# Kernel tuning notes

Measured on AMD Instinct MI355X. Metric: run time of the kernel, lower is better.

## Reference

```python
import jax, jax.numpy as jnp
import numpy as np

DIM_V = 512
NUM_HEADS = 8
LN_EPS = 1e-5


def _layernorm(x):
    # LayerNorm over last dim, no affine (simplified_layer_norm=True)
    mu = jnp.mean(x, axis=-1, keepdims=True)
    var = jnp.mean(jnp.square(x - mu), axis=-1, keepdims=True)
    return (x - mu) * jax.lax.rsqrt(var + LN_EPS)


def setup_inputs() -> dict:
    key = jax.random.key(0)
    ks = jax.random.split(key, 12)
    B, Nq, Nk, dQ, dK, dV = 16, 1024, 1024, 512, 512, DIM_V
    s = 0.02
    return {
        "Q": jax.random.normal(ks[0], (B, Nq, dQ), jnp.float32),
        "K": jax.random.normal(ks[1], (B, Nk, dK), jnp.float32),
        "Wq": jax.random.normal(ks[2], (dQ, dV), jnp.float32) * s,
        "bq": jnp.zeros((dV,), jnp.float32),
        "Wk": jax.random.normal(ks[3], (dK, dV), jnp.float32) * s,
        "bk": jnp.zeros((dV,), jnp.float32),
        "Wv": jax.random.normal(ks[4], (dK, dV), jnp.float32) * s,
        "bv": jnp.zeros((dV,), jnp.float32),
        "Wo": jax.random.normal(ks[5], (dV, dV), jnp.float32) * s,
        "bo": jnp.zeros((dV,), jnp.float32),
    }


def reference(Q, K, Wq, bq, Wk, bk, Wv, bv, Wo, bo):
    H = NUM_HEADS
    dh = DIM_V // H
    q = Q @ Wq + bq            # [B, Nq, dV]
    k = K @ Wk + bk            # [B, Nk, dV]
    v = K @ Wv + bv            # [B, Nk, dV]
    B, Nq, _ = q.shape
    Nk = k.shape[1]
    qh = q.reshape(B, Nq, H, dh)
    kh = k.reshape(B, Nk, H, dh)
    vh = v.reshape(B, Nk, H, dh)
    # NOTE: faithful to source — scale by sqrt(dim_V), not sqrt(head_dim)
    scores = jnp.einsum('bqhd,bkhd->bhqk', qh, kh) / jnp.sqrt(jnp.asarray(DIM_V, q.dtype))
    A = jax.nn.softmax(scores, axis=-1)                    # [B, H, Nq, Nk]
    attn = jnp.einsum('bhqk,bkhd->bqhd', A, vh).reshape(B, Nq, DIM_V)
    O = q + attn               # residual with projected Q
    O = _layernorm(O)          # ln0 (no affine)
    O = O + jax.nn.gelu(O @ Wo + bo, approximate=False)
    O = _layernorm(O)          # ln1 (no affine)
    return O
```

## Files before the change

kernel.cpp:

```cpp
#include <hip/hip_runtime.h>
#include <hip/hip_bf16.h>
#include <math.h>

typedef __bf16 bf16;
typedef __bf16 bf16x8 __attribute__((ext_vector_type(8)));
typedef float  f32x4  __attribute__((ext_vector_type(4)));
typedef float  f32x16 __attribute__((ext_vector_type(16)));
typedef unsigned u32x4 __attribute__((ext_vector_type(4)));

#define MFMA16(a,b,c) __builtin_amdgcn_mfma_f32_16x16x32_bf16((a),(b),(c),0,0,0)
#define MFMA32(a,b,c) __builtin_amdgcn_mfma_f32_32x32x16_bf16((a),(b),(c),0,0,0)
#define KSCALE 0.0637587159f

__device__ __forceinline__ void async16p(const void* g, void* l) {
    __builtin_amdgcn_global_load_lds((const __attribute__((address_space(1))) void*)g,
                                     (__attribute__((address_space(3))) void*)l,
                                     16, 0, 0);
}

__device__ __forceinline__ float fexp2(float x) {
#if __has_builtin(__builtin_amdgcn_exp2f)
    return __builtin_amdgcn_exp2f(x);
#else
    return exp2f(x);
#endif
}

__device__ __forceinline__ unsigned pkbf(float a, float b) {
    union { bf16 h[2]; unsigned u; } x;
    x.h[0] = (bf16)a; x.h[1] = (bf16)b; return x.u;
}

__device__ __forceinline__ void plswap(unsigned &a, unsigned &b) {
#if __has_builtin(__builtin_amdgcn_permlane32_swap)
    auto r = __builtin_amdgcn_permlane32_swap((int)a, (int)b, false, false);
    a = (unsigned)r[0]; b = (unsigned)r[1];
#else
    unsigned sa = (unsigned)__shfl_xor((int)a, 32);
    unsigned sb = (unsigned)__shfl_xor((int)b, 32);
    bool hi = (threadIdx.x & 32) != 0;
    unsigned na = hi ? sb : a;
    unsigned nb = hi ? b  : sa;
    a = na; b = nb;
#endif
}

__global__ __launch_bounds__(256) void prep_w_kernel(
    const float* __restrict__ Wq, const float* __restrict__ Wk,
    const float* __restrict__ Wv, const float* __restrict__ Wo,
    bf16* __restrict__ WqT, bf16* __restrict__ WkT,
    bf16* __restrict__ WvT, bf16* __restrict__ WoT)
{
    __shared__ float tile[32][33];
    const int bx = blockIdx.x;
    const float* W; bf16* T;
    switch (bx >> 8) {
      case 0: W=Wq; T=WqT; break;
      case 1: W=Wk; T=WkT; break;
      case 2: W=Wv; T=WvT; break;
      default: W=Wo; T=WoT; break;
    }
    const int rest = bx & 255;
    const int k0 = (rest & 15) * 32, n0 = (rest >> 4) * 32;
    const int tx = threadIdx.x & 31, ty = threadIdx.x >> 5;
    #pragma unroll
    for (int i=0;i<32;i+=8)
        tile[ty+i][tx] = W[(size_t)(k0+ty+i)*512 + n0+tx];
    __syncthreads();
    #pragma unroll
    for (int i=0;i<32;i+=8)
        T[(size_t)(n0+ty+i)*512 + k0+tx] = (bf16)tile[tx][ty+i];
}

__global__ __launch_bounds__(256) void csum_kernel(
    const float* __restrict__ Wo, float* __restrict__ csum)
{
    const int n = blockIdx.x*256 + threadIdx.x;
    float s = 0.f;
    #pragma unroll 8
    for (int k=0;k<512;k++) s += Wo[(size_t)k*512 + n];
    csum[n] = s;
}

__global__ __launch_bounds__(256, 2) void gemm_proj_kernel(
    const float* __restrict__ Qf, const float* __restrict__ Kf,
    const bf16* __restrict__ WqT, const bf16* __restrict__ WkT,
    const bf16* __restrict__ WvT,
    const float* __restrict__ bq, const float* __restrict__ bk,
    const float* __restrict__ bv,
    bf16* __restrict__ qbb, bf16* __restrict__ kbb, bf16* __restrict__ vT)
{
    __shared__ __align__(16) char smem[65536];
    float* As32 = (float*)smem;
    bf16*  Bs   = (bf16*)(smem + 32768);
    bf16*  Lt   = (bf16*)smem;

    const int x = blockIdx.x;
    const bool isQ = (x < 256);
    int m0, n0;
    const float* A; const bf16 *BT0, *BT1; const float *bb0, *bb1;
    if (isQ) {
        m0 = (x >> 1) * 128; n0 = (x & 1) * 128;
        A = Qf; BT0 = WqT + (size_t)n0*512; BT1 = WqT + (size_t)(n0+256)*512;
        bb0 = bq + n0; bb1 = bq + n0 + 256;
    } else {
        int r = x - 256;
        m0 = (r >> 2) * 128; n0 = (r & 3) * 128;
        A = Kf; BT0 = WkT + (size_t)n0*512; BT1 = WvT + (size_t)n0*512;
        bb0 = bk + n0; bb1 = bv + n0;
    }

    const int tid = threadIdx.x;
    const int lane = tid & 63, wave = tid >> 6;
    const int qd = lane >> 4, lr = lane & 15;
    const int wm = (wave & 1) * 64, wn = (wave >> 1) * 64;

    const float* gA = A + (size_t)(m0 + (tid>>3))*512 + (((tid&7)^((tid>>3)&7))*4);
    const int bgr = ((tid & 3) ^ ((tid >> 3) & 3)) * 8;
    const bf16* gB0 = BT0 + (size_t)(tid>>2)*512 + bgr;
    const bf16* gB1 = BT1 + (size_t)(tid>>2)*512 + bgr;

    f32x4 acc[2][4][4];
    #pragma unroll
    for (int p=0;p<2;p++)
      #pragma unroll
      for (int i=0;i<4;i++)
        #pragma unroll
        for (int j=0;j<4;j++) acc[p][i][j] = (f32x4){0,0,0,0};

    auto stage = [&](int buf, int k0) {
        float* lA = As32 + buf*4096 + wave*256;
        #pragma unroll
        for (int i=0;i<4;i++)
            async16p(gA + k0 + (size_t)i*32*512, lA + i*1024);
        bf16* lB0 = Bs + buf*8192 + wave*512;
        async16p(gB0 + k0,                  lB0);
        async16p(gB0 + k0 + (size_t)64*512, lB0 + 2048);
        bf16* lB1 = Bs + buf*8192 + 4096 + wave*512;
        async16p(gB1 + k0,                  lB1);
        async16p(gB1 + k0 + (size_t)64*512, lB1 + 2048);
    };

    stage(0, 0);
    for (int t = 0; t < 16; ++t) {
        const int cur = t & 1;
        __builtin_amdgcn_sched_barrier(0);
        __builtin_amdgcn_s_barrier();
        if (t < 15) {
            stage(cur ^ 1, (t+1)*32);
            asm volatile("s_waitcnt vmcnt(8)" ::: "memory");
        } else {
            asm volatile("s_waitcnt vmcnt(0)" ::: "memory");
        }
        __builtin_amdgcn_s_barrier();

        const float* Ab = As32 + cur*4096;
        const bf16*  Bb = Bs   + cur*8192;
        bf16x8 af[4], bfr[2][4];
        #pragma unroll
        for (int mi=0;mi<4;mi++) {
            int row = wm + mi*16 + lr;
            f32x4 f0 = *(f32x4*)(Ab + row*32 + (((qd*2  )^(lr&7))*4));
            f32x4 f1 = *(f32x4*)(Ab + row*32 + (((qd*2+1)^(lr&7))*4));
            bf16x8 a;
            a[0]=(bf16)f0[0]; a[1]=(bf16)f0[1]; a[2]=(bf16)f0[2]; a[3]=(bf16)f0[3];
            a[4]=(bf16)f1[0]; a[5]=(bf16)f1[1]; a[6]=(bf16)f1[2]; a[7]=(bf16)f1[3];
            af[mi] = a;
        }
        #pragma unroll
        for (int p=0;p<2;p++)
          #pragma unroll
          for (int ni=0;ni<4;ni++)
            bfr[p][ni] = *(bf16x8*)(Bb + p*4096 + (wn+ni*16+lr)*32
                                       + ((qd^((lr>>1)&3))*8));
        #pragma unroll
        for (int p=0;p<2;p++)
          #pragma unroll
          for (int mi=0;mi<4;mi++)
            #pragma unroll
            for (int ni=0;ni<4;ni++)
              acc[p][mi][ni] = MFMA16(af[mi], bfr[p][ni], acc[p][mi][ni]);
    }

    if (isQ) {
        #pragma unroll
        for (int p=0;p<2;p++) {
            const float* bb = p ? bb1 : bb0;
            #pragma unroll
            for (int ni=0;ni<4;ni++) {
                int nl = wn + ni*16 + lr;
                int n = n0 + p*256 + nl;
                float bv0 = bb[nl];
                #pragma unroll
                for (int mi=0;mi<4;mi++) {
                    int mb = m0 + wm + mi*16 + qd*4;
                    #pragma unroll
                    for (int r=0;r<4;r++)
                        qbb[(size_t)(mb+r)*512 + n] = (bf16)(acc[p][mi][ni][r] + bv0);
                }
            }
        }
    } else {
        #pragma unroll
        for (int ni=0;ni<4;ni++) {
            int nl = wn + ni*16 + lr;
            int n = n0 + nl;
            float bv0 = bb0[nl];
            #pragma unroll
            for (int mi=0;mi<4;mi++) {
                int mb = m0 + wm + mi*16 + qd*4;
                #pragma unroll
                for (int r=0;r<4;r++)
                    kbb[(size_t)(mb+r)*512 + n] = (bf16)((acc[0][mi][ni][r] + bv0)*KSCALE);
            }
        }
        const int b = m0 >> 10, tok0 = m0 & 1023;
        const int row = tid >> 2, ch = tid & 3;
        #pragma unroll
        for (int half = 0; half < 2; ++half) {
            __syncthreads();
            if ((wn >> 6) == half) {
                #pragma unroll
                for (int ni=0;ni<4;ni++) {
                    int nl = ni*16 + lr;
                    float bvv = bb1[half*64 + nl];
                    #pragma unroll
                    for (int mi=0;mi<4;mi++)
                      #pragma unroll
                      for (int r=0;r<4;r++) {
                        int col = wm + mi*16 + qd*4 + r;
                        Lt[nl*128 + ((((col>>3)^(nl&7))<<3) | (col&7))]
                            = (bf16)(acc[1][mi][ni][r] + bvv);
                      }
                }
            }
            __syncthreads();
            const int h = (n0 >> 6) + half;
            bf16* dst = vT + ((size_t)((b*8 + h)*64 + row))*1024 + tok0 + ch*32;
            #pragma unroll
            for (int s=0;s<4;s++) {
                int g = (ch*4 + s) ^ (row & 7);
                *(uint4*)(dst + s*8) = *(uint4*)(Lt + row*128 + g*8);
            }
        }
    }
}

__global__ __launch_bounds__(256, 4) void attn_kernel(
    const bf16* __restrict__ qb, const bf16* __restrict__ kb,
    const bf16* __restrict__ vT, bf16* __restrict__ attnb)
{
    const int x = blockIdx.x;
    const int qt = x >> 7, h = x & 7, b = (x & 127) >> 3;
    const int tid = threadIdx.x, lane = tid & 63, wave = tid >> 6;
    const int l = lane & 31, hi = lane >> 5;
    const int q0w = qt*128 + wave*32;

    __shared__ __align__(16) bf16 kv[2][2][4096];
    __shared__ float ls[4][32];

    bf16x8 aq[4];
    {
        const bf16* qrow = qb + ((size_t)(b*1024 + q0w + l))*512 + h*64 + hi*8;
        #pragma unroll
        for (int st=0; st<4; ++st) aq[st] = *(const bf16x8*)(qrow + st*16);
    }

    const int srow = lane >> 3;
    const int sgA  = (lane & 7) ^ srow ^ wave;
    const int sgB  = sgA ^ 4;
    const bf16* kg0 = kb + ((size_t)(b*1024 + wave*8 + srow))*512      + h*64 + sgA*8;
    const bf16* kg1 = kb + ((size_t)(b*1024 + wave*8 + srow + 32))*512 + h*64 + sgB*8;
    const bf16* vg0 = vT + ((size_t)((b*8 + h)*64 + wave*8 + srow))*1024      + sgA*8;
    const bf16* vg1 = vT + ((size_t)((b*8 + h)*64 + wave*8 + srow + 32))*1024 + sgB*8;

    auto stage = [&](int buf, int t) {
        const size_t ko = (size_t)t*64*512;
        async16p(kg0 + ko,     &kv[buf][0][wave*512]);
        async16p(kg1 + ko,     &kv[buf][0][2048 + wave*512]);
        async16p(vg0 + t*64,   &kv[buf][1][wave*512]);
        async16p(vg1 + t*64,   &kv[buf][1][2048 + wave*512]);
    };

    f32x16 accO[2];
    accO[0] = (f32x16)0.f; accO[1] = (f32x16)0.f;
    float lsum = 0.f;
    const int kx = (l & 7) ^ (l >> 3);

    stage(0, 0);
    for (int t=0; t<16; ++t) {
        const int cur = t & 1;
        __builtin_amdgcn_sched_barrier(0);
        __builtin_amdgcn_s_barrier();
        if (t < 15) {
            stage(cur ^ 1, t + 1);
            asm volatile("s_waitcnt vmcnt(4)" ::: "memory");
        } else {
            asm volatile("s_waitcnt vmcnt(0)" ::: "memory");
        }
        __builtin_amdgcn_s_barrier();

        const bf16* Ks = kv[cur][0];
        const bf16* Vs = kv[cur][1];

        u32x4 paf[4];
        #pragma unroll
        for (int kb2=0; kb2<2; ++kb2) {
            f32x16 sT = (f32x16)0.f;
            __builtin_amdgcn_s_setprio(1);
            #pragma unroll
            for (int st=0; st<4; ++st) {
                bf16x8 kf = *(const bf16x8*)(Ks + (kb2*32 + l)*64
                               + (((st*2 + hi) ^ kx ^ (kb2<<2))*8));
                sT = MFMA32(kf, aq[st], sT);
            }
            __builtin_amdgcn_s_setprio(0);
            unsigned u[8];
            #pragma unroll
            for (int m=0; m<8; ++m) {
                float e0 = fexp2(sT[2*m]);
                float e1 = fexp2(sT[2*m+1]);
                lsum += e0 + e1;
                u[m] = pkbf(e0, e1);
            }
            #pragma unroll
            for (int sb=0; sb<2; ++sb) {
                unsigned a0=u[4*sb], a1=u[4*sb+1], a2=u[4*sb+2], a3=u[4*sb+3];
                plswap(a0, a2);
                plswap(a1, a3);
                paf[kb2*2 + sb] = (u32x4){a0, a1, a2, a3};
            }
        }
        __builtin_amdgcn_s_setprio(1);
        #pragma unroll
        for (int db=0; db<2; ++db) {
            f32x16 a = accO[db];
            #pragma unroll
            for (int st=0; st<4; ++st) {
                bf16x8 vf = *(const bf16x8*)(Vs + (db*32 + l)*64
                               + (((st*2 + hi) ^ kx ^ (db<<2))*8));
                u32x4 pp = paf[st];
                bf16x8 pf = *(bf16x8*)&pp;
                a = MFMA32(pf, vf, a);
            }
            accO[db] = a;
        }
        __builtin_amdgcn_s_setprio(0);
    }

    lsum += __shfl_xor(lsum, 32);
    ls[wave][l] = lsum;
    __syncthreads();

    #pragma unroll
    for (int g=0; g<4; ++g) {
        f32x4 lv = *(const f32x4*)(&ls[wave][g*8 + hi*4]);
        f32x4 inv;
        #pragma unroll
        for (int i=0;i<4;i++) inv[i] = 1.f / lv[i];
        #pragma unroll
        for (int db=0; db<2; ++db) {
            #pragma unroll
            for (int i=0;i<4;i++) {
                int r = g*4 + i;
                int qrow = q0w + g*8 + hi*4 + i;
                size_t idx = ((size_t)(b*1024 + qrow))*512 + h*64 + db*32 + l;
                float o = accO[db][r] * inv[i] + (float)qb[idx];
                attnb[idx] = (bf16)o;
            }
        }
    }
}

__global__ __launch_bounds__(256) void ln_stats_kernel(
    const bf16* __restrict__ attnb, float2* __restrict__ stats)
{
    const int wave = threadIdx.x >> 6, lane = threadIdx.x & 63;
    const int row = blockIdx.x*4 + wave;
    const size_t base = (size_t)row*512 + lane*8;
    bf16x8 av = *(const bf16x8*)(attnb + base);
    float x[8];
    #pragma unroll
    for (int i=0;i<8;i++) x[i] = (float)av[i];
    float s1 = 0.f, s2 = 0.f;
    #pragma unroll
    for (int i=0;i<8;i++){ s1 += x[i]; s2 += x[i]*x[i]; }
    #pragma unroll
    for (int off=1; off<64; off<<=1) { s1 += __shfl_xor(s1, off); s2 += __shfl_xor(s2, off); }
    float mu  = s1 * (1.f/512.f);
    float var = s2 * (1.f/512.f) - mu*mu;
    float rstd = rsqrtf(var + 1e-5f);
    if (lane == 0) stats[row] = make_float2(mu, rstd);
}

__global__ __launch_bounds__(256, 4) void gemm_o_kernel(
    const bf16* __restrict__ attnb, const bf16* __restrict__ WoT,
    const float* __restrict__ bo, const float* __restrict__ csum,
    const float2* __restrict__ stats, bf16* __restrict__ xb)
{
    __shared__ __align__(16) char smem[24576];
    bf16* As = (bf16*)smem;
    bf16* Bs = (bf16*)(smem + 8192);
    const int m0 = blockIdx.x * 64, n0 = blockIdx.y * 128;
    const int tid = threadIdx.x;
    const int lane = tid & 63, wave = tid >> 6;
    const int qd = lane >> 4, lr = lane & 15;
    const int wm = (wave & 1) * 32, wn = (wave >> 1) * 64;

    const int bgr = ((tid & 3) ^ ((tid >> 3) & 3)) * 8;
    const bf16* gA = attnb + (size_t)(m0 + (tid>>2))*512 + bgr;
    const bf16* gB = WoT   + (size_t)(n0 + (tid>>2))*512 + bgr;

    f32x4 acc[2][4];
    #pragma unroll
    for (int i=0;i<2;i++)
      #pragma unroll
      for (int j=0;j<4;j++) acc[i][j] = (f32x4){0,0,0,0};

    auto stage = [&](int buf, int k0) {
        async16p(gA + k0,                  As + buf*2048 + wave*512);
        bf16* lB = Bs + buf*4096 + wave*512;
        async16p(gB + k0,                  lB);
        async16p(gB + k0 + (size_t)64*512, lB + 2048);
    };

    stage(0, 0);
    for (int t = 0; t < 16; ++t) {
        const int cur = t & 1;
        __builtin_amdgcn_sched_barrier(0);
        __builtin_amdgcn_s_barrier();
        if (t < 15) {
            stage(cur ^ 1, (t+1)*32);
            asm volatile("s_waitcnt vmcnt(3)" ::: "memory");
        } else {
            asm volatile("s_waitcnt vmcnt(0)" ::: "memory");
        }
        __builtin_amdgcn_s_barrier();

        const bf16* Ab = As + cur*2048;
        const bf16* Bb = Bs + cur*4096;
        bf16x8 af[2], bfr[4];
        #pragma unroll
        for (int mi=0;mi<2;mi++)
            af[mi] = *(bf16x8*)(Ab + (wm+mi*16+lr)*32 + ((qd^((lr>>1)&3))*8));
        #pragma unroll
        for (int ni=0;ni<4;ni++)
            bfr[ni] = *(bf16x8*)(Bb + (wn+ni*16+lr)*32 + ((qd^((lr>>1)&3))*8));
        #pragma unroll
        for (int mi=0;mi<2;mi++)
          #pragma unroll
          for (int ni=0;ni<4;ni++)
            acc[mi][ni] = MFMA16(af[mi], bfr[ni], acc[mi][ni]);
    }

    float csn[4], bon[4];
    #pragma unroll
    for (int ni=0;ni<4;ni++) {
        int n = n0 + wn + ni*16 + lr;
        csn[ni] = csum[n];
        bon[ni] = bo[n];
    }
    #pragma unroll
    for (int mi=0;mi<2;mi++) {
        #pragma unroll
        for (int r=0;r<4;r++) {
            int row = m0 + wm + mi*16 + qd*4 + r;
            float2 st = stats[row];
            float mu = st.x, rstd = st.y;
            #pragma unroll
            for (int ni=0;ni<4;ni++) {
                int n = n0 + wn + ni*16 + lr;
                float g = rstd*acc[mi][ni][r] - rstd*mu*csn[ni] + bon[ni];
                float gelu = 0.5f * g * (1.f + erff(g * 0.70710678118654752f));
                size_t idx = (size_t)row*512 + n;
                float lnx = ((float)attnb[idx] - mu) * rstd;
                xb[idx] = (bf16)(lnx + gelu);
            }
        }
    }
}

__global__ __launch_bounds__(256) void ln1_kernel(
    const bf16* __restrict__ xb, float* __restrict__ out)
{
    const int wave = threadIdx.x >> 6, lane = threadIdx.x & 63;
    const int row = blockIdx.x*4 + wave;
    const size_t base = (size_t)row*512 + lane*8;
    bf16x8 xv = *(const bf16x8*)(xb + base);
    float x[8];
    #pragma unroll
    for (int i=0;i<8;i++) x[i] = (float)xv[i];
    float s1 = 0.f, s2 = 0.f;
    #pragma unroll
    for (int i=0;i<8;i++){ s1 += x[i]; s2 += x[i]*x[i]; }
    #pragma unroll
    for (int off=1; off<64; off<<=1) { s1 += __shfl_xor(s1, off); s2 += __shfl_xor(s2, off); }
    float mu  = s1 * (1.f/512.f);
    float var = s2 * (1.f/512.f) - mu*mu;
    float rstd = rsqrtf(var + 1e-5f);
    float4 o0 = {(x[0]-mu)*rstd,(x[1]-mu)*rstd,(x[2]-mu)*rstd,(x[3]-mu)*rstd};
    float4 o1 = {(x[4]-mu)*rstd,(x[5]-mu)*rstd,(x[6]-mu)*rstd,(x[7]-mu)*rstd};
    *(float4*)(out + base)     = o0;
    *(float4*)(out + base + 4) = o1;
}

extern "C" void kernel_launch(void* const* d_in, const int* in_sizes, int n_in,
                              void* d_out, int out_size, void* d_ws, size_t ws_size,
                              hipStream_t stream)
{
    (void)in_sizes; (void)n_in; (void)out_size; (void)ws_size;
    const float* Q  = (const float*)d_in[0];
    const float* K  = (const float*)d_in[1];
    const float* Wq = (const float*)d_in[2];
    const float* bq = (const float*)d_in[3];
    const float* Wk = (const float*)d_in[4];
    const float* bk = (const float*)d_in[5];
    const float* Wv = (const float*)d_in[6];
    const float* bv = (const float*)d_in[7];
    const float* Wo = (const float*)d_in[8];
    const float* bo = (const float*)d_in[9];
    float* out = (float*)d_out;

    const size_t nTok = (size_t)16*1024*512;
    char* p = (char*)d_ws;
    auto alloc = [&](size_t bytes)->char* {
        char* r = p; p += (bytes + 255) & ~(size_t)255; return r;
    };
    bf16*   WqT   = (bf16*)alloc(512*512*2);
    bf16*   WkT   = (bf16*)alloc(512*512*2);
    bf16*   WvT   = (bf16*)alloc(512*512*2);
    bf16*   WoT   = (bf16*)alloc(512*512*2);
    bf16*   qbb   = (bf16*)alloc(nTok*2);
    bf16*   kbb   = (bf16*)alloc(nTok*2);
    bf16*   vT    = (bf16*)alloc(nTok*2);
    bf16*   attnb = (bf16*)alloc(nTok*2);
    bf16*   xb    = (bf16*)alloc(nTok*2);
    float*  csum  = (float*)alloc(512*4);
    float2* stats = (float2*)alloc(16384*8);

    prep_w_kernel<<<1024, 256, 0, stream>>>(Wq, Wk, Wv, Wo, WqT, WkT, WvT, WoT);
    csum_kernel<<<2, 256, 0, stream>>>(Wo, csum);
    gemm_proj_kernel<<<768, 256, 0, stream>>>(Q, K, WqT, WkT, WvT,
                                              bq, bk, bv, qbb, kbb, vT);
    attn_kernel<<<dim3(1024), 256, 0, stream>>>(qbb, kbb, vT, attnb);
    ln_stats_kernel<<<4096, 256, 0, stream>>>(attnb, stats);
    gemm_o_kernel<<<dim3(256,4), 256, 0, stream>>>(attnb, WoT, bo, csum, stats, xb);
    ln1_kernel<<<4096, 256, 0, stream>>>(xb, out);
}
```

Baseline: 265.7 us.

## Fuse column-sum into weight prep and split projection GEMM into per-output tiles

The Wo column-sum kernel is folded into the weight transpose kernel using block reductions and atomicAdd, with a memset clearing the buffer first. The projection GEMM now computes a single 128x128 output tile per block over 1536 blocks instead of paired Q halves or K/V outputs. B fragments are read straight from global memory into registers, which halves LDS use and lets occupancy rise to three blocks per CU. In exchange, the fp32 activation tile is re-read for every output slice (K is loaded twice), and the B loads are no longer staged through LDS.

```diff
diff --git a/kernel.cpp b/kernel.cpp
--- a/kernel.cpp
+++ b/kernel.cpp
@@ -49,7 +49,8 @@
     const float* __restrict__ Wq, const float* __restrict__ Wk,
     const float* __restrict__ Wv, const float* __restrict__ Wo,
     bf16* __restrict__ WqT, bf16* __restrict__ WkT,
-    bf16* __restrict__ WvT, bf16* __restrict__ WoT)
+    bf16* __restrict__ WvT, bf16* __restrict__ WoT,
+    float* __restrict__ csum)
 {
     __shared__ float tile[32][33];
     const int bx = blockIdx.x;
@@ -63,26 +64,31 @@
     const int rest = bx & 255;
     const int k0 = (rest & 15) * 32, n0 = (rest >> 4) * 32;
     const int tx = threadIdx.x & 31, ty = threadIdx.x >> 5;
-    #pragma unroll
-    for (int i=0;i<32;i+=8)
-        tile[ty+i][tx] = W[(size_t)(k0+ty+i)*512 + n0+tx];
+    float sacc = 0.f;
+    #pragma unroll
+    for (int i=0;i<32;i+=8) {
+        float v = W[(size_t)(k0+ty+i)*512 + n0+tx];
+        tile[ty+i][tx] = v;
+        sacc += v;
+    }
     __syncthreads();
     #pragma unroll
     for (int i=0;i<32;i+=8)
         T[(size_t)(n0+ty+i)*512 + k0+tx] = (bf16)tile[tx][ty+i];
-}
-
-__global__ __launch_bounds__(256) void csum_kernel(
-    const float* __restrict__ Wo, float* __restrict__ csum)
-{
-    const int n = blockIdx.x*256 + threadIdx.x;
-    float s = 0.f;
-    #pragma unroll 8
-    for (int k=0;k<512;k++) s += Wo[(size_t)k*512 + n];
-    csum[n] = s;
-}
-
-__global__ __launch_bounds__(256, 2) void gemm_proj_kernel(
+    if ((bx >> 8) == 3) {
+        __syncthreads();
+        tile[ty][tx] = sacc;
+        __syncthreads();
+        if (ty == 0) {
+            float s = 0.f;
+            #pragma unroll
+            for (int j=0;j<8;j++) s += tile[j][tx];
+            atomicAdd(&csum[n0+tx], s);
+        }
+    }
+}
+
+__global__ __launch_bounds__(256, 3) void gemm_proj_kernel(
     const float* __restrict__ Qf, const float* __restrict__ Kf,
     const bf16* __restrict__ WqT, const bf16* __restrict__ WkT,
     const bf16* __restrict__ WvT,
@@ -90,25 +96,17 @@
     const float* __restrict__ bv,
     bf16* __restrict__ qbb, bf16* __restrict__ kbb, bf16* __restrict__ vT)
 {
-    __shared__ __align__(16) char smem[65536];
+    __shared__ __align__(16) char smem[32768];
     float* As32 = (float*)smem;
-    bf16*  Bs   = (bf16*)(smem + 32768);
     bf16*  Lt   = (bf16*)smem;
 
     const int x = blockIdx.x;
-    const bool isQ = (x < 256);
-    int m0, n0;
-    const float* A; const bf16 *BT0, *BT1; const float *bb0, *bb1;
-    if (isQ) {
-        m0 = (x >> 1) * 128; n0 = (x & 1) * 128;
-        A = Qf; BT0 = WqT + (size_t)n0*512; BT1 = WqT + (size_t)(n0+256)*512;
-        bb0 = bq + n0; bb1 = bq + n0 + 256;
-    } else {
-        int r = x - 256;
-        m0 = (r >> 2) * 128; n0 = (r & 3) * 128;
-        A = Kf; BT0 = WkT + (size_t)n0*512; BT1 = WvT + (size_t)n0*512;
-        bb0 = bk + n0; bb1 = bv + n0;
-    }
+    const int z = x >> 9;
+    const int r = x & 511;
+    const int m0 = (r >> 2) * 128, n0 = (r & 3) * 128;
+    const float* A  = (z == 0) ? Qf : Kf;
+    const bf16*  BT = (z == 0) ? WqT : (z == 1) ? WkT : WvT;
+    const float* bb = (z == 0) ? bq  : (z == 1) ? bk  : bv;
 
     const int tid = threadIdx.x;
     const int lane = tid & 63, wave = tid >> 6;
@@ -116,29 +114,19 @@
     const int wm = (wave & 1) * 64, wn = (wave >> 1) * 64;
 
     const float* gA = A + (size_t)(m0 + (tid>>3))*512 + (((tid&7)^((tid>>3)&7))*4);
-    const int bgr = ((tid & 3) ^ ((tid >> 3) & 3)) * 8;
-    const bf16* gB0 = BT0 + (size_t)(tid>>2)*512 + bgr;
-    const bf16* gB1 = BT1 + (size_t)(tid>>2)*512 + bgr;
-
-    f32x4 acc[2][4][4];
-    #pragma unroll
-    for (int p=0;p<2;p++)
+    const bf16*  gB = BT + (size_t)(n0 + wn + lr)*512 + qd*8;
+
+    f32x4 acc[4][4];
+    #pragma unroll
+    for (int i=0;i<4;i++)
       #pragma unroll
-      for (int i=0;i<4;i++)
-        #pragma unroll
-        for (int j=0;j<4;j++) acc[p][i][j] = (f32x4){0,0,0,0};
+      for (int j=0;j<4;j++) acc[i][j] = (f32x4){0,0,0,0};
 
     auto stage = [&](int buf, int k0) {
         float* lA = As32 + buf*4096 + wave*256;
         #pragma unroll
         for (int i=0;i<4;i++)
             async16p(gA + k0 + (size_t)i*32*512, lA + i*1024);
-        bf16* lB0 = Bs + buf*8192 + wave*512;
-        async16p(gB0 + k0,                  lB0);
-        async16p(gB0 + k0 + (size_t)64*512, lB0 + 2048);
-        bf16* lB1 = Bs + buf*8192 + 4096 + wave*512;
-        async16p(gB1 + k0,                  lB1);
-        async16p(gB1 + k0 + (size_t)64*512, lB1 + 2048);
     };
 
     stage(0, 0);
@@ -146,17 +134,20 @@
         const int cur = t & 1;
         __builtin_amdgcn_sched_barrier(0);
         __builtin_amdgcn_s_barrier();
+        bf16x8 bfr[4];
+        #pragma unroll
+        for (int ni=0;ni<4;ni++)
+            bfr[ni] = *(const bf16x8*)(gB + (size_t)ni*16*512 + t*32);
         if (t < 15) {
             stage(cur ^ 1, (t+1)*32);
             asm volatile("s_waitcnt vmcnt(8)" ::: "memory");
         } else {
-            asm volatile("s_waitcnt vmcnt(0)" ::: "memory");
+            asm volatile("s_waitcnt vmcnt(4)" ::: "memory");
         }
         __builtin_amdgcn_s_barrier();
 
         const float* Ab = As32 + cur*4096;
-        const bf16*  Bb = Bs   + cur*8192;
-        bf16x8 af[4], bfr[2][4];
+        bf16x8 af[4];
         #pragma unroll
         for (int mi=0;mi<4;mi++) {
             int row = wm + mi*16 + lr;
@@ -168,52 +159,39 @@
             af[mi] = a;
         }
         #pragma unroll
-        for (int p=0;p<2;p++)
+        for (int mi=0;mi<4;mi++)
           #pragma unroll
           for (int ni=0;ni<4;ni++)
-            bfr[p][ni] = *(bf16x8*)(Bb + p*4096 + (wn+ni*16+lr)*32
-                                       + ((qd^((lr>>1)&3))*8));
-        #pragma unroll
-        for (int p=0;p<2;p++)
-          #pragma unroll
-          for (int mi=0;mi<4;mi++)
-            #pragma unroll
-            for (int ni=0;ni<4;ni++)
-              acc[p][mi][ni] = MFMA16(af[mi], bfr[p][ni], acc[p][mi][ni]);
-    }
-
-    if (isQ) {
-        #pragma unroll
-        for (int p=0;p<2;p++) {
-            const float* bb = p ? bb1 : bb0;
-            #pragma unroll
-            for (int ni=0;ni<4;ni++) {
-                int nl = wn + ni*16 + lr;
-                int n = n0 + p*256 + nl;
-                float bv0 = bb[nl];
-                #pragma unroll
-                for (int mi=0;mi<4;mi++) {
-                    int mb = m0 + wm + mi*16 + qd*4;
-                    #pragma unroll
-                    for (int r=0;r<4;r++)
-                        qbb[(size_t)(mb+r)*512 + n] = (bf16)(acc[p][mi][ni][r] + bv0);
-                }
-            }
-        }
-    } else {
+            acc[mi][ni] = MFMA16(af[mi], bfr[ni], acc[mi][ni]);
+    }
+
+    if (z == 0) {
         #pragma unroll
         for (int ni=0;ni<4;ni++) {
-            int nl = wn + ni*16 + lr;
-            int n = n0 + nl;
-            float bv0 = bb0[nl];
+            int n = n0 + wn + ni*16 + lr;
+            float bv0 = bb[n - n0];
             #pragma unroll
             for (int mi=0;mi<4;mi++) {
                 int mb = m0 + wm + mi*16 + qd*4;
                 #pragma unroll
-                for (int r=0;r<4;r++)
-                    kbb[(size_t)(mb+r)*512 + n] = (bf16)((acc[0][mi][ni][r] + bv0)*KSCALE);
-            }
-        }
+                for (int r2=0;r2<4;r2++)
+                    qbb[(size_t)(mb+r2)*512 + n] = (bf16)(acc[mi][ni][r2] + bv0);
+            }
+        }
+    } else if (z == 1) {
+        #pragma unroll
+        for (int ni=0;ni<4;ni++) {
+            int n = n0 + wn + ni*16 + lr;
+            float bv0 = bb[n - n0];
+            #pragma unroll
+            for (int mi=0;mi<4;mi++) {
+                int mb = m0 + wm + mi*16 + qd*4;
+                #pragma unroll
+                for (int r2=0;r2<4;r2++)
+                    kbb[(size_t)(mb+r2)*512 + n] = (bf16)((acc[mi][ni][r2] + bv0)*KSCALE);
+            }
+        }
+    } else {
         const int b = m0 >> 10, tok0 = m0 & 1023;
         const int row = tid >> 2, ch = tid & 3;
         #pragma unroll
@@ -223,14 +201,15 @@
                 #pragma unroll
                 for (int ni=0;ni<4;ni++) {
                     int nl = ni*16 + lr;
-                    float bvv = bb1[half*64 + nl];
+                    float bvv = bb[half*64 + (wn & 63) + nl - (wn & 63)];
+                    bvv = bb[half*64 + nl];
                     #pragma unroll
                     for (int mi=0;mi<4;mi++)
                       #pragma unroll
-                      for (int r=0;r<4;r++) {
-                        int col = wm + mi*16 + qd*4 + r;
+                      for (int r2=0;r2<4;r2++) {
+                        int col = wm + mi*16 + qd*4 + r2;
                         Lt[nl*128 + ((((col>>3)^(nl&7))<<3) | (col&7))]
-                            = (bf16)(acc[1][mi][ni][r] + bvv);
+                            = (bf16)(acc[mi][ni][r2] + bvv);
                       }
                 }
             }
@@ -538,10 +517,10 @@
     float*  csum  = (float*)alloc(512*4);
     float2* stats = (float2*)alloc(16384*8);
 
-    prep_w_kernel<<<1024, 256, 0, stream>>>(Wq, Wk, Wv, Wo, WqT, WkT, WvT, WoT);
-    csum_kernel<<<2, 256, 0, stream>>>(Wo, csum);
-    gemm_proj_kernel<<<768, 256, 0, stream>>>(Q, K, WqT, WkT, WvT,
-                                              bq, bk, bv, qbb, kbb, vT);
+    hipMemsetAsync(csum, 0, 512*sizeof(float), stream);
+    prep_w_kernel<<<1024, 256, 0, stream>>>(Wq, Wk, Wv, Wo, WqT, WkT, WvT, WoT, csum);
+    gemm_proj_kernel<<<1536, 256, 0, stream>>>(Q, K, WqT, WkT, WvT,
+                                               bq, bk, bv, qbb, kbb, vT);
     attn_kernel<<<dim3(1024), 256, 0, stream>>>(qbb, kbb, vT, attnb);
     ln_stats_kernel<<<4096, 256, 0, stream>>>(attnb, stats);
     gemm_o_kernel<<<dim3(256,4), 256, 0, stream>>>(attnb, WoT, bo, csum, stats, xb);
```

Result: slower. 276.9 us (+4.2%).
